# Optimization experiments

Measured on AMD Instinct MI355X. Metric: run time of the kernel, lower is better.

## Reference

```python
import jax, jax.numpy as jnp
import numpy as np

IO, H, S, N = 64, 1024, 512, 64

def setup_inputs() -> dict:
    key = jax.random.key(0)
    ks = jax.random.split(key, 6)
    scale = 0.05  # keep activations in a sane range for tanh/softmax
    return {
        "states": jax.random.normal(ks[0], (N, S, H), jnp.float32) * scale,
        "output_set": jax.random.normal(ks[1], (IO, H), jnp.float32) * scale,
        "Wo": jax.random.normal(ks[2], (2 * H, H), jnp.float32) * scale,
        "bo": jax.random.normal(ks[3], (H,), jnp.float32) * scale,
        "Wc": jax.random.normal(ks[4], (IO * H, IO), jnp.float32) * scale,
        "bc": jax.random.normal(ks[5], (IO,), jnp.float32) * scale,
    }

def reference(states, output_set, Wo, bo, Wc, bc):
    # Batched over the n_states Python loop of the original module.
    # attn scores: output_set [io,h] x states [n,s,h] -> [n,io,s]
    attn = jnp.einsum('ih,nsh->nis', output_set, states)
    attn = jax.nn.softmax(attn, axis=-1)  # softmax over context (sm_over_context=True)
    mix = jnp.einsum('nis,nsh->nih', attn, states)            # [n,io,h]
    out = jnp.broadcast_to(output_set[None], mix.shape)       # [n,io,h]
    combined = jnp.concatenate([mix, out], axis=-1)           # [n,io,2h]
    o = combined @ Wo + bo                                    # linear_out: 2h -> h
    logits = jnp.tanh(o).reshape(o.shape[0], -1) @ Wc + bc    # C: io*h -> io
    return logits
```

## Files before the change

kernel.cpp:

```cpp
#include <hip/hip_runtime.h>
#include <hip/hip_bf16.h>

#define IOdim 64
#define Hdim  1024
#define Sdim  512
#define Nbat  64

typedef __bf16 bf16x8_t __attribute__((ext_vector_type(8)));
typedef float  f32x4_t  __attribute__((ext_vector_type(4)));

#define MFMA16(a, b, c) __builtin_amdgcn_mfma_f32_16x16x32_bf16((a), (b), (c), 0, 0, 0)

__device__ __forceinline__ unsigned short f2bf(float f) {
    return __builtin_bit_cast(unsigned short, (__bf16)f);
}
__device__ __forceinline__ bf16x8_t cvt8(float4 p0, float4 p1) {
    bf16x8_t b;
    b[0] = (__bf16)p0.x; b[1] = (__bf16)p0.y; b[2] = (__bf16)p0.z; b[3] = (__bf16)p0.w;
    b[4] = (__bf16)p1.x; b[5] = (__bf16)p1.y; b[6] = (__bf16)p1.z; b[7] = (__bf16)p1.w;
    return b;
}
__device__ __forceinline__ void async16(const void* g, void* l) {
    __builtin_amdgcn_global_load_lds(
        (const __attribute__((address_space(1))) void*)g,
        (__attribute__((address_space(3))) void*)l, 16, 0, 0);
}

__global__ __launch_bounds__(256) void cvt_kernel(const float* __restrict__ in,
                                                  unsigned short* __restrict__ outp,
                                                  int nElem) {
    int idx = blockIdx.x * 256 + threadIdx.x;
    if (idx < nElem) outp[idx] = f2bf(in[idx]);
}

__global__ __launch_bounds__(256) void transpose_cvt(const float* __restrict__ in,
                                                     unsigned short* __restrict__ outp,
                                                     int R, int C) {
    __shared__ float tile[32][33];
    int c0 = blockIdx.x * 32, r0 = blockIdx.y * 32;
    int tx = threadIdx.x, ty = threadIdx.y;
#pragma unroll
    for (int i = 0; i < 4; i++) {
        int r = ty + i * 8;
        tile[r][tx] = in[(size_t)(r0 + r) * C + c0 + tx];
    }
    __syncthreads();
#pragma unroll
    for (int i = 0; i < 4; i++) {
        int r = ty + i * 8;
        outp[(size_t)(c0 + r) * R + r0 + tx] = f2bf(tile[tx][r]);
    }
}

__global__ __launch_bounds__(256) void scores_kernel(const float* __restrict__ states,
                                                     const unsigned short* __restrict__ osb,
                                                     float* __restrict__ attnf) {
    int n = blockIdx.y;
    int tid = threadIdx.x, lane = tid & 63, w = tid >> 6;
    int col = lane & 15, quad = lane >> 4;
    int sh = w & 1, ih = w >> 1;
    int s = blockIdx.x * 32 + sh * 16 + col;
    const float* srow = states + (size_t)(n * Sdim + s) * Hdim + quad * 8;
    const unsigned short* ap = osb + (size_t)(ih * 32 + col) * Hdim + quad * 8;
    f32x4_t acc0 = {0,0,0,0}, acc1 = {0,0,0,0};
    float4 pc0[2], pc1[2];
    bf16x8_t pA0[2], pA1[2];
#pragma unroll
    for (int t = 0; t < 2; t++) {
        pc0[t] = *(const float4*)(srow + t * 32);
        pc1[t] = *(const float4*)(srow + t * 32 + 4);
        pA0[t] = *(const bf16x8_t*)(ap + t * 32);
        pA1[t] = *(const bf16x8_t*)(ap + 16 * Hdim + t * 32);
    }
#pragma unroll 4
    for (int kc = 0; kc < Hdim; kc += 32) {
        int p = (kc >> 5) & 1;
        bf16x8_t b = cvt8(pc0[p], pc1[p]);
        acc0 = MFMA16(pA0[p], b, acc0);
        acc1 = MFMA16(pA1[p], b, acc1);
        int kn = kc + 64;
        if (kn < Hdim) {
            pc0[p] = *(const float4*)(srow + kn);
            pc1[p] = *(const float4*)(srow + kn + 4);
            pA0[p] = *(const bf16x8_t*)(ap + kn);
            pA1[p] = *(const bf16x8_t*)(ap + 16 * Hdim + kn);
        }
    }
    f32x4_t accs[2] = {acc0, acc1};
    float* ob = attnf + (size_t)(n * IOdim) * Sdim + blockIdx.x * 32 + sh * 16 + col;
#pragma unroll
    for (int t = 0; t < 2; t++)
#pragma unroll
        for (int r = 0; r < 4; r++) {
            int i = ih * 32 + t * 16 + quad * 4 + r;
            ob[i * Sdim] = accs[t][r];
        }
}

__global__ __launch_bounds__(256) void softmax_kernel(const float* __restrict__ attnf,
                                                      unsigned short* __restrict__ attnb) {
    int row = blockIdx.x * 4 + (threadIdx.x >> 6);
    int lane = threadIdx.x & 63;
    const float* p = attnf + (size_t)row * Sdim + lane * 8;
    float4 v0 = ((const float4*)p)[0];
    float4 v1 = ((const float4*)p)[1];
    float v[8] = {v0.x, v0.y, v0.z, v0.w, v1.x, v1.y, v1.z, v1.w};
    float m = v[0];
#pragma unroll
    for (int j = 1; j < 8; j++) m = fmaxf(m, v[j]);
#pragma unroll
    for (int off = 32; off > 0; off >>= 1) m = fmaxf(m, __shfl_xor(m, off));
    float sum = 0.f;
#pragma unroll
    for (int j = 0; j < 8; j++) { v[j] = __expf(v[j] - m); sum += v[j]; }
#pragma unroll
    for (int off = 32; off > 0; off >>= 1) sum += __shfl_xor(sum, off);
    float inv = 1.0f / sum;
    union { unsigned short u[8]; uint4 q; } res;
#pragma unroll
    for (int j = 0; j < 8; j++) res.u[j] = f2bf(v[j] * inv);
    *(uint4*)(attnb + (size_t)row * Sdim + lane * 8) = res.q;
}

__global__ __launch_bounds__(256) void mix_kernel(const float* __restrict__ states,
                                                  const unsigned short* __restrict__ attnb,
                                                  unsigned short* __restrict__ mixb) {
    __shared__ unsigned short Tlds[64 * 72];
    int n = blockIdx.y, h0 = blockIdx.x * 64;
    int tid = threadIdx.x, lane = tid & 63, g = tid >> 6;
    int col = lane & 15, quad = lane >> 4;
    f32x4_t acc0 = {0,0,0,0}, acc1 = {0,0,0,0}, acc2 = {0,0,0,0}, acc3 = {0,0,0,0};
    const unsigned short* ap = attnb + (size_t)(n * IOdim + col) * Sdim + quad * 8;
    const float* sbase = states + (size_t)n * Sdim * Hdim + h0 + lane;
    float cur[16];
#pragma unroll
    for (int rep = 0; rep < 16; rep++) cur[rep] = sbase[(size_t)(g * 16 + rep) * Hdim];
    for (int sc = 0; sc < Sdim; sc += 64) {
        union { unsigned short u[16]; uint4 q[2]; } pk;
#pragma unroll
        for (int rep = 0; rep < 16; rep++) pk.u[rep] = f2bf(cur[rep]);
        if (sc) __syncthreads();
        *(uint4*)(Tlds + lane * 72 + g * 16)     = pk.q[0];
        *(uint4*)(Tlds + lane * 72 + g * 16 + 8) = pk.q[1];
        if (sc + 64 < Sdim) {
#pragma unroll
            for (int rep = 0; rep < 16; rep++)
                cur[rep] = sbase[(size_t)(sc + 64 + g * 16 + rep) * Hdim];
        }
        __syncthreads();
#pragma unroll
        for (int ks = 0; ks < 64; ks += 32) {
            bf16x8_t b  = *(const bf16x8_t*)(Tlds + (g * 16 + col) * 72 + ks + quad * 8);
            bf16x8_t a0 = *(const bf16x8_t*)(ap + sc + ks);
            bf16x8_t a1 = *(const bf16x8_t*)(ap + 16 * Sdim + sc + ks);
            bf16x8_t a2 = *(const bf16x8_t*)(ap + 32 * Sdim + sc + ks);
            bf16x8_t a3 = *(const bf16x8_t*)(ap + 48 * Sdim + sc + ks);
            acc0 = MFMA16(a0, b, acc0);
            acc1 = MFMA16(a1, b, acc1);
            acc2 = MFMA16(a2, b, acc2);
            acc3 = MFMA16(a3, b, acc3);
        }
    }
    f32x4_t accs[4] = {acc0, acc1, acc2, acc3};
    int h = h0 + g * 16 + col;
#pragma unroll
    for (int ai = 0; ai < 4; ai++)
#pragma unroll
        for (int r = 0; r < 4; r++) {
            int i = ai * 16 + quad * 4 + r;
            mixb[(size_t)(n * IOdim + i) * Hdim + h] = f2bf(accs[ai][r]);
        }
}

__global__ __launch_bounds__(256) void out_gemm(const unsigned short* __restrict__ mixb,
                                                const unsigned short* __restrict__ osb,
                                                const unsigned short* __restrict__ woT,
                                                const float* __restrict__ bo,
                                                unsigned short* __restrict__ tb) {
    __shared__ unsigned short Ald[128 * 32];
    __shared__ unsigned short Bld[64 * 32];
    int h0 = blockIdx.x * 64, r0 = blockIdx.y * 128;
    int tid = threadIdx.x, lane = tid & 63, w = tid >> 6;
    int col = lane & 15, quad = lane >> 4;
    int wx = w & 1, wy = w >> 1;
    int rowX = tid >> 2, seg = tid & 3;
    f32x4_t acc[4][2] = {};
    const unsigned short* m1 = mixb + (size_t)(r0 + rowX) * Hdim + seg * 8;
    const unsigned short* m2 = mixb + (size_t)(r0 + rowX + 64) * Hdim + seg * 8;
    const unsigned short* o1 = osb + (size_t)rowX * Hdim + seg * 8;
    const unsigned short* w1 = woT + (size_t)(h0 + rowX) * 2048 + seg * 8;
    unsigned short* lA1 = Ald + (size_t)tid * 8;
    unsigned short* lA2 = Ald + (size_t)(tid + 256) * 8;
    unsigned short* lB1 = Bld + (size_t)tid * 8;
    for (int kc = 0; kc < 2048; kc += 32) {
        if (kc < 1024) {
            async16(m1 + kc, lA1);
            async16(m2 + kc, lA2);
        } else {
            int k2 = kc - 1024;
            async16(o1 + k2, lA1);
            async16(o1 + k2, lA2);
        }
        async16(w1 + kc, lB1);
        __syncthreads();
        bf16x8_t af[4], bfr[2];
#pragma unroll
        for (int mi = 0; mi < 4; mi++)
            af[mi] = *(const bf16x8_t*)(Ald + (wy * 64 + mi * 16 + col) * 32 + quad * 8);
#pragma unroll
        for (int ni = 0; ni < 2; ni++)
            bfr[ni] = *(const bf16x8_t*)(Bld + (wx * 32 + ni * 16 + col) * 32 + quad * 8);
#pragma unroll
        for (int mi = 0; mi < 4; mi++)
#pragma unroll
            for (int ni = 0; ni < 2; ni++)
                acc[mi][ni] = MFMA16(af[mi], bfr[ni], acc[mi][ni]);
        __syncthreads();
    }
#pragma unroll
    for (int ni = 0; ni < 2; ni++) {
        int h = h0 + wx * 32 + ni * 16 + col;
        float bov = bo[h];
#pragma unroll
        for (int mi = 0; mi < 4; mi++)
#pragma unroll
            for (int r = 0; r < 4; r++) {
                int rr = r0 + wy * 64 + mi * 16 + quad * 4 + r;
                tb[(size_t)rr * Hdim + h] = f2bf(tanhf(acc[mi][ni][r] + bov));
            }
    }
}

__global__ __launch_bounds__(256) void final_gemm(const unsigned short* __restrict__ tb,
                                                  const unsigned short* __restrict__ wcT,
                                                  float* __restrict__ partials) {
    int kc0 = blockIdx.x * 128;
    int tid = threadIdx.x, lane = tid & 63, g = tid >> 6;
    int col = lane & 15, quad = lane >> 4;
    f32x4_t acc0 = {0,0,0,0}, acc1 = {0,0,0,0}, acc2 = {0,0,0,0}, acc3 = {0,0,0,0};
    const unsigned short* ap = tb + (size_t)col * 65536 + kc0 + quad * 8;
    const unsigned short* bp = wcT + (size_t)(g * 16 + col) * 65536 + kc0 + quad * 8;
    bf16x8_t B[2], A0[2], A1[2], A2[2], A3[2];
#pragma unroll
    for (int t = 0; t < 2; t++) {
        B[t]  = *(const bf16x8_t*)(bp + t * 32);
        A0[t] = *(const bf16x8_t*)(ap + t * 32);
        A1[t] = *(const bf16x8_t*)(ap + (size_t)16 * 65536 + t * 32);
        A2[t] = *(const bf16x8_t*)(ap + (size_t)32 * 65536 + t * 32);
        A3[t] = *(const bf16x8_t*)(ap + (size_t)48 * 65536 + t * 32);
    }
#pragma unroll
    for (int c = 0; c < 4; c++) {
        int p = c & 1;
        acc0 = MFMA16(A0[p], B[p], acc0);
        acc1 = MFMA16(A1[p], B[p], acc1);
        acc2 = MFMA16(A2[p], B[p], acc2);
        acc3 = MFMA16(A3[p], B[p], acc3);
        if (c + 2 < 4) {
            int kn = (c + 2) * 32;
            B[p]  = *(const bf16x8_t*)(bp + kn);
            A0[p] = *(const bf16x8_t*)(ap + kn);
            A1[p] = *(const bf16x8_t*)(ap + (size_t)16 * 65536 + kn);
            A2[p] = *(const bf16x8_t*)(ap + (size_t)32 * 65536 + kn);
            A3[p] = *(const bf16x8_t*)(ap + (size_t)48 * 65536 + kn);
        }
    }
    f32x4_t accs[4] = {acc0, acc1, acc2, acc3};
    int j = g * 16 + col;
    float* pb = partials + blockIdx.x * 4096;
#pragma unroll
    for (int ai = 0; ai < 4; ai++)
#pragma unroll
        for (int r = 0; r < 4; r++) {
            int nn = ai * 16 + quad * 4 + r;
            pb[nn * 64 + j] = accs[ai][r];
        }
}

__global__ __launch_bounds__(256) void reduce_kernel(const float* __restrict__ partials,
                                                     const float* __restrict__ bc,
                                                     float* __restrict__ out) {
    int idx = blockIdx.x * 256 + threadIdx.x;
    float s = bc[idx & 63];
#pragma unroll 8
    for (int b = 0; b < 512; b++) s += partials[b * 4096 + idx];
    out[idx] = s;
}

extern "C" void kernel_launch(void* const* d_in, const int* in_sizes, int n_in,
                              void* d_out, int out_size, void* d_ws, size_t ws_size,
                              hipStream_t stream) {
    const float* states     = (const float*)d_in[0];
    const float* output_set = (const float*)d_in[1];
    const float* Wo         = (const float*)d_in[2];
    const float* bo         = (const float*)d_in[3];
    const float* Wc         = (const float*)d_in[4];
    const float* bc         = (const float*)d_in[5];
    float* out = (float*)d_out;

    char* ws = (char*)d_ws;
    float*          attnf = (float*)ws;
    float*          parts = (float*)ws;
    unsigned short* attnb = (unsigned short*)(ws + (8u  << 20));
    unsigned short* mixb  = (unsigned short*)(ws + (12u << 20));
    unsigned short* tb    = (unsigned short*)(ws + (20u << 20));
    unsigned short* woT   = (unsigned short*)(ws + (28u << 20));
    unsigned short* osb   = (unsigned short*)(ws + (32u << 20));
    unsigned short* wcT   = (unsigned short*)(ws + (32u << 20) + (1u << 18));

    cvt_kernel<<<dim3(IOdim * Hdim / 256), dim3(256), 0, stream>>>(output_set, osb, IOdim * Hdim);
    transpose_cvt<<<dim3(Hdim / 32, 2048 / 32), dim3(32, 8), 0, stream>>>(Wo, woT, 2048, Hdim);
    transpose_cvt<<<dim3(64 / 32, 65536 / 32), dim3(32, 8), 0, stream>>>(Wc, wcT, 65536, 64);
    scores_kernel<<<dim3(Sdim / 32, Nbat), dim3(256), 0, stream>>>(states, osb, attnf);
    softmax_kernel<<<dim3(Nbat * IOdim / 4), dim3(256), 0, stream>>>(attnf, attnb);
    mix_kernel<<<dim3(Hdim / 64, Nbat), dim3(256), 0, stream>>>(states, attnb, mixb);
    out_gemm<<<dim3(Hdim / 64, Nbat * IOdim / 128), dim3(256), 0, stream>>>(mixb, osb, woT, bo, tb);
    final_gemm<<<dim3(512), dim3(256), 0, stream>>>(tb, wcT, parts);
    reduce_kernel<<<dim3(16), dim3(256), 0, stream>>>(parts, bc, out);
}
```

Before: 355.2 us.

## Stage scores GEMM tiles in LDS via async global-to-LDS loads

The scores kernel now computes a 64x64 tile (all 64 io rows by 64 positions) per block, staging states and output_set chunks in shared memory with async global_load_lds copies. Each block reads a 64-wide K chunk once and reuses it across four MFMA row tiles, instead of every wave streaming its own fragments from global memory. This halves the grid size and adds two barriers per K step with no double buffering, so load latency is no longer overlapped with compute.

```diff
diff --git a/kernel.cpp b/kernel.cpp
--- a/kernel.cpp
+++ b/kernel.cpp
@@ -55,45 +55,45 @@
 __global__ __launch_bounds__(256) void scores_kernel(const float* __restrict__ states,
                                                      const unsigned short* __restrict__ osb,
                                                      float* __restrict__ attnf) {
-    int n = blockIdx.y;
+    __shared__ float Bst[64 * 64];
+    __shared__ unsigned short Ast[64 * 64];
+    int n = blockIdx.y, s0 = blockIdx.x * 64;
     int tid = threadIdx.x, lane = tid & 63, w = tid >> 6;
     int col = lane & 15, quad = lane >> 4;
-    int sh = w & 1, ih = w >> 1;
-    int s = blockIdx.x * 32 + sh * 16 + col;
-    const float* srow = states + (size_t)(n * Sdim + s) * Hdim + quad * 8;
-    const unsigned short* ap = osb + (size_t)(ih * 32 + col) * Hdim + quad * 8;
-    f32x4_t acc0 = {0,0,0,0}, acc1 = {0,0,0,0};
-    float4 pc0[2], pc1[2];
-    bf16x8_t pA0[2], pA1[2];
-#pragma unroll
-    for (int t = 0; t < 2; t++) {
-        pc0[t] = *(const float4*)(srow + t * 32);
-        pc1[t] = *(const float4*)(srow + t * 32 + 4);
-        pA0[t] = *(const bf16x8_t*)(ap + t * 32);
-        pA1[t] = *(const bf16x8_t*)(ap + 16 * Hdim + t * 32);
-    }
-#pragma unroll 4
-    for (int kc = 0; kc < Hdim; kc += 32) {
-        int p = (kc >> 5) & 1;
-        bf16x8_t b = cvt8(pc0[p], pc1[p]);
-        acc0 = MFMA16(pA0[p], b, acc0);
-        acc1 = MFMA16(pA1[p], b, acc1);
-        int kn = kc + 64;
-        if (kn < Hdim) {
-            pc0[p] = *(const float4*)(srow + kn);
-            pc1[p] = *(const float4*)(srow + kn + 4);
-            pA0[p] = *(const bf16x8_t*)(ap + kn);
-            pA1[p] = *(const bf16x8_t*)(ap + 16 * Hdim + kn);
-        }
-    }
-    f32x4_t accs[2] = {acc0, acc1};
-    float* ob = attnf + (size_t)(n * IOdim) * Sdim + blockIdx.x * 32 + sh * 16 + col;
-#pragma unroll
-    for (int t = 0; t < 2; t++)
+    const float* bsrc = states + ((size_t)(n * Sdim + s0 + (tid >> 4)) << 10) + (tid & 15) * 4;
+    const unsigned short* asrc = osb + ((size_t)(tid >> 3) << 10) + (tid & 7) * 8;
+    float* bdst = Bst + tid * 4;
+    unsigned short* adst = Ast + tid * 8;
+    f32x4_t acc[4] = {};
+    for (int kc = 0; kc < Hdim; kc += 64) {
+#pragma unroll
+        for (int j = 0; j < 4; j++)
+            async16(bsrc + ((size_t)j << 14) + kc, bdst + j * 1024);
+#pragma unroll
+        for (int j = 0; j < 2; j++)
+            async16(asrc + ((size_t)j << 15) + kc, adst + j * 2048);
+        __syncthreads();
+#pragma unroll
+        for (int kk = 0; kk < 2; kk++) {
+            const float* bp = Bst + (w * 16 + col) * 64 + kk * 32 + quad * 8;
+            float4 f0 = *(const float4*)bp;
+            float4 f1 = *(const float4*)(bp + 4);
+            bf16x8_t bfrag = cvt8(f0, f1);
+#pragma unroll
+            for (int a = 0; a < 4; a++) {
+                bf16x8_t afrag = *(const bf16x8_t*)(Ast + (a * 16 + col) * 64 + kk * 32 + quad * 8);
+                acc[a] = MFMA16(afrag, bfrag, acc[a]);
+            }
+        }
+        __syncthreads();
+    }
+    float* ob = attnf + (size_t)(n * IOdim) * Sdim + s0 + w * 16 + col;
+#pragma unroll
+    for (int a = 0; a < 4; a++)
 #pragma unroll
         for (int r = 0; r < 4; r++) {
-            int i = ih * 32 + t * 16 + quad * 4 + r;
-            ob[i * Sdim] = accs[t][r];
+            int i = a * 16 + quad * 4 + r;
+            ob[(size_t)i * Sdim] = acc[a][r];
         }
 }
 
@@ -311,7 +311,7 @@
     cvt_kernel<<<dim3(IOdim * Hdim / 256), dim3(256), 0, stream>>>(output_set, osb, IOdim * Hdim);
     transpose_cvt<<<dim3(Hdim / 32, 2048 / 32), dim3(32, 8), 0, stream>>>(Wo, woT, 2048, Hdim);
     transpose_cvt<<<dim3(64 / 32, 65536 / 32), dim3(32, 8), 0, stream>>>(Wc, wcT, 65536, 64);
-    scores_kernel<<<dim3(Sdim / 32, Nbat), dim3(256), 0, stream>>>(states, osb, attnf);
+    scores_kernel<<<dim3(Sdim / 64, Nbat), dim3(256), 0, stream>>>(states, osb, attnf);
     softmax_kernel<<<dim3(Nbat * IOdim / 4), dim3(256), 0, stream>>>(attnf, attnb);
     mix_kernel<<<dim3(Hdim / 64, Nbat), dim3(256), 0, stream>>>(states, attnb, mixb);
     out_gemm<<<dim3(Hdim / 64, Nbat * IOdim / 128), dim3(256), 0, stream>>>(mixb, osb, woT, bo, tb);
```

Measured after the change: 343.7 us. 3.2% less time.
